# Optimization experiments

Hardware: AMD Instinct MI355X
Metric: run time of the kernel (lower is better)

The kernel has to match this reference:

```python
import jax, jax.numpy as jnp
import numpy as np

B, N, H, E, P = 2, 20000, 128, 200000, 3


def _mlp2(x, w1, b1, w2, b2):
    # Linear -> SiLU -> Linear
    return jax.nn.silu(x @ w1 + b1) @ w2 + b2


def setup_inputs() -> dict:
    key = jax.random.key(0)
    ks = iter(jax.random.split(key, 40))
    def nrm(shape, s=0.05):
        return jax.random.normal(next(ks), shape, dtype=jnp.float32) * s
    inp = {
        "features": jax.random.normal(next(ks), (B, N, H), dtype=jnp.float32),
        "positions": jax.random.normal(next(ks), (B, N, P), dtype=jnp.float32),
        "edge_index_up": jax.random.randint(next(ks), (2, E), 0, N, dtype=jnp.int32),
        "edge_index_down": jax.random.randint(next(ks), (2, E), 0, N, dtype=jnp.int32),
        "degree_up": jax.random.uniform(next(ks), (N,), minval=1.0, maxval=32.0, dtype=jnp.float32),
        "degree_down": jax.random.uniform(next(ks), (N,), minval=1.0, maxval=32.0, dtype=jnp.float32),
    }
    for name in ("up", "down"):
        inp[f"w_msg1_{name}"] = nrm((2 * H + 1, H)); inp[f"b_msg1_{name}"] = jnp.zeros((H,), jnp.float32)
        inp[f"w_msg2_{name}"] = nrm((H, H));         inp[f"b_msg2_{name}"] = jnp.zeros((H,), jnp.float32)
        inp[f"w_pos1_{name}"] = nrm((H, H));         inp[f"b_pos1_{name}"] = jnp.zeros((H,), jnp.float32)
        inp[f"w_pos2_{name}"] = nrm((H, 1));         inp[f"b_pos2_{name}"] = jnp.zeros((1,), jnp.float32)
    inp["w_upd1"] = nrm((2 * H, H)); inp["b_upd1"] = jnp.zeros((H,), jnp.float32)
    inp["w_upd2"] = nrm((H, H));     inp["b_upd2"] = jnp.zeros((H,), jnp.float32)
    return inp


def reference(features, positions, edge_index_up, edge_index_down, degree_up, degree_down,
              w_msg1_up, b_msg1_up, w_msg2_up, b_msg2_up,
              w_pos1_up, b_pos1_up, w_pos2_up, b_pos2_up,
              w_msg1_down, b_msg1_down, w_msg2_down, b_msg2_down,
              w_pos1_down, b_pos1_down, w_pos2_down, b_pos2_down,
              w_upd1, b_upd1, w_upd2, b_upd2):
    n_neighborhoods = 2
    msg_acc = jnp.zeros_like(features)
    pos_upd = jnp.zeros_like(positions)
    neighborhoods = [
        (edge_index_up, degree_up,
         (w_msg1_up, b_msg1_up, w_msg2_up, b_msg2_up),
         (w_pos1_up, b_pos1_up, w_pos2_up, b_pos2_up)),
        (edge_index_down, degree_down,
         (w_msg1_down, b_msg1_down, w_msg2_down, b_msg2_down),
         (w_pos1_down, b_pos1_down, w_pos2_down, b_pos2_down)),
    ]
    for edge_index, degree, msg_p, pos_p in neighborhoods:
        src, dst = edge_index[0], edge_index[1]
        h_src = features[:, src, :]                     # [B, E, H] gather
        h_dst = features[:, dst, :]                     # [B, E, H] gather
        rel_pos = positions[:, src, :] - positions[:, dst, :]  # [B, E, P]
        dist = jnp.linalg.norm(rel_pos, axis=-1, keepdims=True)  # [B, E, 1]
        msg_input = jnp.concatenate([h_src, h_dst, dist], axis=-1)  # [B, E, 2H+1]
        messages = _mlp2(msg_input, *msg_p)             # [B, E, H]
        agg = jnp.zeros_like(features).at[:, dst, :].add(messages)  # scatter-add over dim 1
        agg = agg / jnp.clip(degree, 1.0, None)[None, :, None]
        msg_acc = msg_acc + agg
        weights = jnp.tanh(_mlp2(messages, *pos_p))     # [B, E, 1]
        pos_upd = pos_upd + jnp.zeros_like(positions).at[:, dst, :].add(weights * rel_pos)
    feat_update = _mlp2(jnp.concatenate([features, msg_acc], axis=-1), w_upd1, b_upd1, w_upd2, b_upd2)
    updated_features = features + feat_update
    updated_positions = positions + pos_upd / n_neighborhoods
    return updated_features, updated_positions
```

## Files before the change

### kernel.cpp

```cpp
#include <hip/hip_runtime.h>

#define BB 2
#define NN 20000
#define HH 128
#define EE 200000
#define EBLK 3125
#define NBLK 79

typedef unsigned short u16;
typedef __attribute__((ext_vector_type(4))) float f32x4;
typedef __bf16 bf16x8 __attribute__((ext_vector_type(8)));

#define MFMA(a, b, c) __builtin_amdgcn_mfma_f32_16x16x32_bf16((a), (b), (c), 0, 0, 0)

__device__ __forceinline__ float bf2f(u16 u) {
    union { unsigned int i; float f; } v; v.i = ((unsigned int)u) << 16; return v.f;
}
__device__ __forceinline__ u16 f2bf(float f) {
    union { __bf16 h; u16 u; } v; v.h = (__bf16)f; return v.u;
}
__device__ __forceinline__ float silu_f(float z) { return z / (1.f + __expf(-z)); }

__global__ void detect_kernel(const u16* __restrict__ f, int* __restrict__ flag) {
    int tid = threadIdx.x;
    u16 v = f[tid * 2];
    int e = (v >> 7) & 0xFF;
    int ok = (e >= 101 && e <= 143) ? 1 : 0;
    __shared__ int cnt;
    if (tid == 0) cnt = 0;
    __syncthreads();
    atomicAdd(&cnt, ok);
    __syncthreads();
    if (tid == 0) *flag = (cnt < 200) ? 1 : 0;
}

#define CTOT 5461776
struct P24 { const void* p[24]; };

__global__ __launch_bounds__(256) void canon_kernel(P24 ptrs, const int* __restrict__ flag,
                                                    u16* __restrict__ canon) {
    static const int off[25] = {
        0, 5120000, 5240000, 5260000, 5280000, 5312896, 5313024, 5329408,
        5329536, 5345920, 5346048, 5346176, 5346184, 5379080, 5379208, 5395592,
        5395720, 5412104, 5412232, 5412360, 5412368, 5445136, 5445264, 5461648,
        5461776 };
    static const int rsz[24] = {
        5120000, 120000, 20000, 20000,
        32896, 128, 16384, 128, 16384, 128, 128, 1,
        32896, 128, 16384, 128, 16384, 128, 128, 1,
        32768, 128, 16384, 128 };
    int i = blockIdx.x * 256 + threadIdx.x;
    if (i >= CTOT) return;
    int t = 0;
#pragma unroll 1
    while (i >= off[t + 1]) ++t;
    int j = i - off[t];
    u16 v;
    if (j >= rsz[t]) v = 0;
    else if (*flag) v = f2bf(((const float*)ptrs.p[t])[j]);
    else v = ((const u16*)ptrs.p[t])[j];
    canon[i] = v;
}

#define FTOT 180224
struct P8 { const u16* w[8]; };

__global__ __launch_bounds__(256) void make_frag_all(P8 ws, u16* __restrict__ fbase) {
    static const int foff[9] = { 0, 32768, 49152, 65536, 98304, 114688, 131072, 163840, 180224 };
    int i = blockIdx.x * 256 + threadIdx.x;
    if (i >= FTOT) return;
    int t = 0;
#pragma unroll 1
    while (i >= foff[t + 1]) ++t;
    int j = i - foff[t];
    int jj = j & 7, lane = (j >> 3) & 63, nt = (j >> 9) & 7, kt = j >> 12;
    int k = kt * 32 + ((lane >> 4) * 8) + jj;
    int n = nt * 16 + (lane & 15);
    fbase[i] = ws.w[t][k * 128 + n];
}

__global__ void count2_kernel(const int* __restrict__ eu, const int* __restrict__ ed,
                              int* __restrict__ cu, int* __restrict__ cd) {
    int e = blockIdx.x * 256 + threadIdx.x;
    if (e < EE) atomicAdd(&cu[eu[EE + e]], 1);
    else { e -= EE; if (e < EE) atomicAdd(&cd[ed[EE + e]], 1); }
}

struct SP { const int* cnt[2]; int* cur[2]; int* bsum[2]; };

__global__ __launch_bounds__(256) void scan1_kernel(SP p) {
    int half = blockIdx.x / NBLK;
    int b = blockIdx.x - half * NBLK;
    int t = threadIdx.x;
    int i = b * 256 + t;
    __shared__ int buf[256];
    int v = (i < NN) ? p.cnt[half][i] : 0;
    buf[t] = v;
    __syncthreads();
    for (int s = 1; s < 256; s <<= 1) {
        int x = (t >= s) ? buf[t - s] : 0;
        __syncthreads();
        buf[t] += x;
        __syncthreads();
    }
    if (i < NN) p.cur[half][i] = buf[t] - v;
    if (t == 255) p.bsum[half][b] = buf[255];
}

__global__ __launch_bounds__(256) void scan2_kernel(int* __restrict__ bu, int* __restrict__ bd) {
    __shared__ int buf[2][128];
    int half = threadIdx.x >> 7, t = threadIdx.x & 127;
    int* bs = half ? bd : bu;
    int v = (t < NBLK) ? bs[t] : 0;
    buf[half][t] = v;
    __syncthreads();
    for (int s = 1; s < 128; s <<= 1) {
        int x = (t >= s) ? buf[half][t - s] : 0;
        __syncthreads();
        buf[half][t] += x;
        __syncthreads();
    }
    if (t < NBLK) bs[t] = buf[half][t] - v;
}

__global__ void scan3_kernel(int* __restrict__ cu, const int* __restrict__ bu,
                             int* __restrict__ cd, const int* __restrict__ bd) {
    int i = blockIdx.x * 256 + threadIdx.x;
    if (i < NN) cu[i] += bu[i >> 8];
    else { i -= NN; if (i < NN) cd[i] += bd[i >> 8]; }
}

__global__ void scatter2_kernel(const int* __restrict__ eu, const int* __restrict__ ed,
                                int* __restrict__ cu, int* __restrict__ cd,
                                int* __restrict__ su, int* __restrict__ sd) {
    int e = blockIdx.x * 256 + threadIdx.x;
    if (e < EE) { int p = atomicAdd(&cu[eu[EE + e]], 1); su[p] = e; }
    else { e -= EE; if (e < EE) { int p = atomicAdd(&cd[ed[EE + e]], 1); sd[p] = e; } }
}

struct EP {
    const int* eidx; const int* es; const u16* deg;
    const u16* fW1; const u16* w1last; const u16* bias1;
    const u16* fW2; const u16* bias2;
    const u16* fP1; const u16* biasp1;
    const u16* wp2; const u16* biasp2;
};

__global__ __launch_bounds__(512, 8) void edge_kernel(
    const u16* __restrict__ feat, const u16* __restrict__ posit,
    EP up, EP dn,
    float* __restrict__ msg_acc, float* __restrict__ pos_acc)
{
    const int tid = threadIdx.x;
    const int lane = tid & 63;
    const int wv = tid >> 6;
    const int half = blockIdx.x / (BB * EBLK);
    const int rem = blockIdx.x - half * (BB * EBLK);
    const int bb = rem / EBLK;
    const int s0 = (rem - bb * EBLK) * 64;
    const EP P = half ? dn : up;

    __shared__ u16 sX[64][136];
    __shared__ u16 sY[64][136];
    __shared__ float sRel[64][3];
    __shared__ float sDist[64];
    __shared__ float sInv[64];
    __shared__ int sSrc[64], sDst[64];

    if (tid < 64) {
        int e = P.es[s0 + tid];
        int s = P.eidx[e];
        int d = P.eidx[EE + e];
        sSrc[tid] = s; sDst[tid] = d;
        sInv[tid] = 1.f / fmaxf(bf2f(P.deg[d]), 1.f);
        const u16* ps = posit + ((size_t)bb * NN + s) * 3;
        const u16* pd = posit + ((size_t)bb * NN + d) * 3;
        float dx = bf2f(ps[0]) - bf2f(pd[0]);
        float dy = bf2f(ps[1]) - bf2f(pd[1]);
        float dz = bf2f(ps[2]) - bf2f(pd[2]);
        sRel[tid][0] = dx; sRel[tid][1] = dy; sRel[tid][2] = dz;
        sDist[tid] = sqrtf(dx * dx + dy * dy + dz * dz);
    }
    __syncthreads();

    {
        const int r = tid >> 3, part = tid & 7;
        const uint4* fs = (const uint4*)(feat + ((size_t)bb * NN + sSrc[r]) * HH);
        const uint4* fd = (const uint4*)(feat + ((size_t)bb * NN + sDst[r]) * HH);
        uint4* as = (uint4*)&sX[r][part * 16];
        uint4* ad = (uint4*)&sY[r][part * 16];
#pragma unroll
        for (int i = 0; i < 2; ++i) { as[i] = fs[part * 2 + i]; ad[i] = fd[part * 2 + i]; }
    }
    __syncthreads();

    const int nt = wv;
    const int mrow = lane & 15;
    const int kq = (lane >> 4) * 8;
    const int crow = (lane >> 4) * 4;
    const int ccol = lane & 15;
    const int col = nt * 16 + ccol;

    f32x4 acc[4];
#pragma unroll
    for (int mt = 0; mt < 4; ++mt) acc[mt] = (f32x4){0.f, 0.f, 0.f, 0.f};

#pragma unroll
    for (int kt = 0; kt < 8; ++kt) {
        const u16* Xb = (kt < 4) ? &sX[0][0] : &sY[0][0];
        const int kk = (kt & 3) * 32 + kq;
        bf16x8 bw = *(const bf16x8*)(P.fW1 + (size_t)(((kt * 8 + nt) * 64 + lane) * 8));
#pragma unroll
        for (int mt = 0; mt < 4; ++mt) {
            bf16x8 a = *(const bf16x8*)(Xb + (mt * 16 + mrow) * 136 + kk);
            acc[mt] = MFMA(a, bw, acc[mt]);
        }
    }
    __syncthreads();

    {
        const float wl = bf2f(P.w1last[col]);
        const float bb2 = bf2f(P.bias1[col]);
#pragma unroll
        for (int mt = 0; mt < 4; ++mt) {
#pragma unroll
            for (int r = 0; r < 4; ++r) {
                const int row = mt * 16 + crow + r;
                float z = fmaf(sDist[row], wl, acc[mt][r]) + bb2;
                sX[row][col] = f2bf(silu_f(z));
            }
        }
    }
    __syncthreads();

#pragma unroll
    for (int mt = 0; mt < 4; ++mt) acc[mt] = (f32x4){0.f, 0.f, 0.f, 0.f};
#pragma unroll
    for (int kt = 0; kt < 4; ++kt) {
        const int kk = kt * 32 + kq;
        bf16x8 bw = *(const bf16x8*)(P.fW2 + (size_t)(((kt * 8 + nt) * 64 + lane) * 8));
#pragma unroll
        for (int mt = 0; mt < 4; ++mt) {
            bf16x8 a = *(const bf16x8*)(&sX[0][0] + (mt * 16 + mrow) * 136 + kk);
            acc[mt] = MFMA(a, bw, acc[mt]);
        }
    }
    {
        const float bb2 = bf2f(P.bias2[col]);
#pragma unroll
        for (int mt = 0; mt < 4; ++mt) {
#pragma unroll
            for (int r = 0; r < 4; ++r) {
                const int row = mt * 16 + crow + r;
                sY[row][col] = f2bf(acc[mt][r] + bb2);
            }
        }
    }
    __syncthreads();

#pragma unroll
    for (int mt = 0; mt < 4; ++mt) acc[mt] = (f32x4){0.f, 0.f, 0.f, 0.f};
#pragma unroll
    for (int kt = 0; kt < 4; ++kt) {
        const int kk = kt * 32 + kq;
        bf16x8 bw = *(const bf16x8*)(P.fP1 + (size_t)(((kt * 8 + nt) * 64 + lane) * 8));
#pragma unroll
        for (int mt = 0; mt < 4; ++mt) {
            bf16x8 a = *(const bf16x8*)(&sY[0][0] + (mt * 16 + mrow) * 136 + kk);
            acc[mt] = MFMA(a, bw, acc[mt]);
        }
    }

    {
        const int scol = tid & 127;
        const int r0 = (tid >> 7) * 16;
        float accv = 0.f;
        int dprev = sDst[r0];
        float invprev = sInv[r0];
#pragma unroll 1
        for (int r = r0; r < r0 + 16; ++r) {
            int dcur = sDst[r];
            if (dcur != dprev) {
                unsafeAtomicAdd(&msg_acc[((size_t)bb * NN + dprev) * HH + scol], accv * invprev);
                accv = 0.f; dprev = dcur; invprev = sInv[r];
            }
            accv += bf2f(sY[r][scol]);
        }
        unsafeAtomicAdd(&msg_acc[((size_t)bb * NN + dprev) * HH + scol], accv * invprev);
    }

    {
        const float bb2 = bf2f(P.biasp1[col]);
#pragma unroll
        for (int mt = 0; mt < 4; ++mt) {
#pragma unroll
            for (int r = 0; r < 4; ++r) {
                const int row = mt * 16 + crow + r;
                sX[row][col] = f2bf(silu_f(acc[mt][r] + bb2));
            }
        }
    }
    __syncthreads();

    {
        const int r = tid >> 3, q = tid & 7;
        const unsigned int* t32 = (const unsigned int*)&sX[r][q * 16];
        const unsigned int* w32 = (const unsigned int*)(P.wp2 + q * 16);
        float p = 0.f;
#pragma unroll
        for (int k = 0; k < 8; ++k) {
            unsigned int a = t32[k], b = w32[k];
            union { unsigned int i; float f; } al, ah, bl, bh;
            al.i = a << 16; ah.i = a & 0xffff0000u;
            bl.i = b << 16; bh.i = b & 0xffff0000u;
            p = fmaf(al.f, bl.f, p);
            p = fmaf(ah.f, bh.f, p);
        }
        p += __shfl_xor(p, 1);
        p += __shfl_xor(p, 2);
        p += __shfl_xor(p, 4);
        if (q == 0) {
            float wgt = tanhf(p + bf2f(P.biasp2[0]));
            const size_t pb = ((size_t)bb * NN + sDst[r]) * 3;
            unsafeAtomicAdd(&pos_acc[pb + 0], wgt * sRel[r][0]);
            unsafeAtomicAdd(&pos_acc[pb + 1], wgt * sRel[r][1]);
            unsafeAtomicAdd(&pos_acc[pb + 2], wgt * sRel[r][2]);
        }
    }
}

__global__ __launch_bounds__(256) void update_kernel(
    const u16* __restrict__ feat, const void* __restrict__ rawfeat,
    const float* __restrict__ magg,
    const u16* __restrict__ fU1, const u16* __restrict__ bu1,
    const u16* __restrict__ fU2, const u16* __restrict__ bu2,
    void* __restrict__ outp, const int* __restrict__ flag)
{
    const int tid = threadIdx.x;
    const int lane = tid & 63;
    const int wv = tid >> 6;
    const int row0 = blockIdx.x * 64;
    const int isf = *flag;

    __shared__ u16 sA[64][136];
    __shared__ u16 sB[64][136];

    {
        const uint4* src = (const uint4*)(feat + (size_t)row0 * HH);
        for (int i = tid; i < 1024; i += 256) {
            int r = i >> 4, c = i & 15;
            *(uint4*)&sA[r][c * 8] = src[i];
        }
        const float4* am = (const float4*)(magg) + (size_t)row0 * 32;
        for (int i = tid; i < 2048; i += 256) {
            int r = i >> 5;
            float4 v = am[i];
            int c = (i & 31) * 4;
            sB[r][c + 0] = f2bf(v.x);
            sB[r][c + 1] = f2bf(v.y);
            sB[r][c + 2] = f2bf(v.z);
            sB[r][c + 3] = f2bf(v.w);
        }
    }
    __syncthreads();

    const int nt0 = wv * 2;
    const int mrow = lane & 15;
    const int kq = (lane >> 4) * 8;
    const int crow = (lane >> 4) * 4;
    const int ccol = lane & 15;

    f32x4 acc[4][2];
#pragma unroll
    for (int mt = 0; mt < 4; ++mt) {
        acc[mt][0] = (f32x4){0.f, 0.f, 0.f, 0.f};
        acc[mt][1] = (f32x4){0.f, 0.f, 0.f, 0.f};
    }
#pragma unroll
    for (int kt = 0; kt < 8; ++kt) {
        const u16* Xb = (kt < 4) ? &sA[0][0] : &sB[0][0];
        const int kk = (kt & 3) * 32 + kq;
        bf16x8 bw0 = *(const bf16x8*)(fU1 + (size_t)(((kt * 8 + nt0) * 64 + lane) * 8));
        bf16x8 bw1 = *(const bf16x8*)(fU1 + (size_t)(((kt * 8 + nt0 + 1) * 64 + lane) * 8));
#pragma unroll
        for (int mt = 0; mt < 4; ++mt) {
            bf16x8 a = *(const bf16x8*)(Xb + (mt * 16 + mrow) * 136 + kk);
            acc[mt][0] = MFMA(a, bw0, acc[mt][0]);
            acc[mt][1] = MFMA(a, bw1, acc[mt][1]);
        }
    }
    __syncthreads();

#pragma unroll
    for (int mt = 0; mt < 4; ++mt) {
#pragma unroll
        for (int n2 = 0; n2 < 2; ++n2) {
            const int col = (nt0 + n2) * 16 + ccol;
            const float bb = bf2f(bu1[col]);
#pragma unroll
            for (int r = 0; r < 4; ++r) {
                const int row = mt * 16 + crow + r;
                sB[row][col] = f2bf(silu_f(acc[mt][n2][r] + bb));
            }
        }
    }
    __syncthreads();

#pragma unroll
    for (int mt = 0; mt < 4; ++mt) {
        acc[mt][0] = (f32x4){0.f, 0.f, 0.f, 0.f};
        acc[mt][1] = (f32x4){0.f, 0.f, 0.f, 0.f};
    }
#pragma unroll
    for (int kt = 0; kt < 4; ++kt) {
        const int kk = kt * 32 + kq;
        bf16x8 bw0 = *(const bf16x8*)(fU2 + (size_t)(((kt * 8 + nt0) * 64 + lane) * 8));
        bf16x8 bw1 = *(const bf16x8*)(fU2 + (size_t)(((kt * 8 + nt0 + 1) * 64 + lane) * 8));
#pragma unroll
        for (int mt = 0; mt < 4; ++mt) {
            bf16x8 a = *(const bf16x8*)(&sB[0][0] + (mt * 16 + mrow) * 136 + kk);
            acc[mt][0] = MFMA(a, bw0, acc[mt][0]);
            acc[mt][1] = MFMA(a, bw1, acc[mt][1]);
        }
    }
#pragma unroll
    for (int mt = 0; mt < 4; ++mt) {
#pragma unroll
        for (int n2 = 0; n2 < 2; ++n2) {
            const int col = (nt0 + n2) * 16 + ccol;
            const float bb = bf2f(bu2[col]);
#pragma unroll
            for (int r = 0; r < 4; ++r) {
                const int row = mt * 16 + crow + r;
                const size_t idx = (size_t)(row0 + row) * HH + col;
                if (isf) {
                    float base = ((const float*)rawfeat)[idx];
                    ((float*)outp)[idx] = acc[mt][n2][r] + bb + base;
                } else {
                    float base = bf2f(sA[row][col]);
                    ((u16*)outp)[idx] = f2bf(acc[mt][n2][r] + bb + base);
                }
            }
        }
    }
}

__global__ void pos_out_kernel(const void* __restrict__ rawpos, const u16* __restrict__ cpos,
                               const float* __restrict__ pacc, void* __restrict__ outp,
                               const int* __restrict__ flag)
{
    int i = blockIdx.x * 256 + threadIdx.x;
    if (i >= BB * NN * 3) return;
    if (*flag) {
        float base = ((const float*)rawpos)[i];
        ((float*)outp)[5120000 + i] = base + 0.5f * pacc[i];
    } else {
        float base = bf2f(cpos[i]);
        ((u16*)outp)[5120000 + i] = f2bf(base + 0.5f * pacc[i]);
    }
}

extern "C" void kernel_launch(void* const* d_in, const int* in_sizes, int n_in,
                              void* d_out, int out_size, void* d_ws, size_t ws_size,
                              hipStream_t stream)
{
    float* msg_acc = (float*)d_ws;
    float* pos_acc = (float*)((char*)d_ws + 20480000);
    int*   cnt_up  = (int*)((char*)d_ws + 20960000);
    int*   cnt_dn  = (int*)((char*)d_ws + 21040000);
    const size_t ZERO_BYTES = 21120000;
    int*   cur_up  = (int*)((char*)d_ws + 21120000);
    int*   cur_dn  = (int*)((char*)d_ws + 21200000);
    int*   bsum_up = (int*)((char*)d_ws + 21280000);
    int*   bsum_dn = (int*)((char*)d_ws + 21280400);
    int*   es_up   = (int*)((char*)d_ws + 21280800);
    int*   es_dn   = (int*)((char*)d_ws + 22080800);
    u16*   fbase   = (u16*)((char*)d_ws + 22880800);
    u16*   canon   = (u16*)((char*)d_ws + 23241248);
    int*   flag    = (int*)((char*)d_ws + 34164800);
    if (ws_size < 34164804ULL) return;

    u16* f_m1u = fbase;
    u16* f_m2u = fbase + 32768;
    u16* f_p1u = fbase + 49152;
    u16* f_m1d = fbase + 65536;
    u16* f_m2d = fbase + 98304;
    u16* f_p1d = fbase + 114688;
    u16* f_u1  = fbase + 131072;
    u16* f_u2  = fbase + 163840;

    u16* cfeat = canon;
    u16* cpos  = canon + 5120000;
    u16* cdgu  = canon + 5240000;
    u16* cdgd  = canon + 5260000;
    u16* cm1u  = canon + 5280000;
    u16* cbm1u = canon + 5312896;
    u16* cm2u  = canon + 5313024;
    u16* cbm2u = canon + 5329408;
    u16* cp1u  = canon + 5329536;
    u16* cbp1u = canon + 5345920;
    u16* cp2u  = canon + 5346048;
    u16* cbp2u = canon + 5346176;
    u16* cm1d  = canon + 5346184;
    u16* cbm1d = canon + 5379080;
    u16* cm2d  = canon + 5379208;
    u16* cbm2d = canon + 5395592;
    u16* cp1d  = canon + 5395720;
    u16* cbp1d = canon + 5412104;
    u16* cp2d  = canon + 5412232;
    u16* cbp2d = canon + 5412360;
    u16* cu1   = canon + 5412368;
    u16* cbu1  = canon + 5445136;
    u16* cu2   = canon + 5445264;
    u16* cbu2  = canon + 5461648;

    hipMemsetAsync(d_ws, 0, ZERO_BYTES, stream);

    detect_kernel<<<1, 256, 0, stream>>>((const u16*)d_in[0], flag);

    P24 ptrs;
    ptrs.p[0] = d_in[0];  ptrs.p[1] = d_in[1];  ptrs.p[2] = d_in[4];  ptrs.p[3] = d_in[5];
    ptrs.p[4] = d_in[6];  ptrs.p[5] = d_in[7];  ptrs.p[6] = d_in[8];  ptrs.p[7] = d_in[9];
    ptrs.p[8] = d_in[10]; ptrs.p[9] = d_in[11]; ptrs.p[10] = d_in[12]; ptrs.p[11] = d_in[13];
    ptrs.p[12] = d_in[14]; ptrs.p[13] = d_in[15]; ptrs.p[14] = d_in[16]; ptrs.p[15] = d_in[17];
    ptrs.p[16] = d_in[18]; ptrs.p[17] = d_in[19]; ptrs.p[18] = d_in[20]; ptrs.p[19] = d_in[21];
    ptrs.p[20] = d_in[22]; ptrs.p[21] = d_in[23]; ptrs.p[22] = d_in[24]; ptrs.p[23] = d_in[25];
    canon_kernel<<<(CTOT + 255) / 256, 256, 0, stream>>>(ptrs, flag, canon);

    P8 wsf;
    wsf.w[0] = cm1u; wsf.w[1] = cm2u; wsf.w[2] = cp1u; wsf.w[3] = cm1d;
    wsf.w[4] = cm2d; wsf.w[5] = cp1d; wsf.w[6] = cu1;  wsf.w[7] = cu2;
    make_frag_all<<<(FTOT + 255) / 256, 256, 0, stream>>>(wsf, fbase);

    const int* ei_up = (const int*)d_in[2];
    const int* ei_dn = (const int*)d_in[3];

    count2_kernel<<<(2 * EE + 255) / 256, 256, 0, stream>>>(ei_up, ei_dn, cnt_up, cnt_dn);
    SP sp;
    sp.cnt[0] = cnt_up; sp.cnt[1] = cnt_dn;
    sp.cur[0] = cur_up; sp.cur[1] = cur_dn;
    sp.bsum[0] = bsum_up; sp.bsum[1] = bsum_dn;
    scan1_kernel<<<2 * NBLK, 256, 0, stream>>>(sp);
    scan2_kernel<<<1, 256, 0, stream>>>(bsum_up, bsum_dn);
    scan3_kernel<<<(2 * NN + 255) / 256, 256, 0, stream>>>(cur_up, bsum_up, cur_dn, bsum_dn);
    scatter2_kernel<<<(2 * EE + 255) / 256, 256, 0, stream>>>(ei_up, ei_dn, cur_up, cur_dn,
                                                              es_up, es_dn);

    EP up, dn;
    up.eidx = ei_up; up.es = es_up; up.deg = cdgu;
    up.fW1 = f_m1u; up.w1last = cm1u + 256 * 128; up.bias1 = cbm1u;
    up.fW2 = f_m2u; up.bias2 = cbm2u;
    up.fP1 = f_p1u; up.biasp1 = cbp1u;
    up.wp2 = cp2u;  up.biasp2 = cbp2u;
    dn.eidx = ei_dn; dn.es = es_dn; dn.deg = cdgd;
    dn.fW1 = f_m1d; dn.w1last = cm1d + 256 * 128; dn.bias1 = cbm1d;
    dn.fW2 = f_m2d; dn.bias2 = cbm2d;
    dn.fP1 = f_p1d; dn.biasp1 = cbp1d;
    dn.wp2 = cp2d;  dn.biasp2 = cbp2d;

    edge_kernel<<<2 * BB * EBLK, 512, 0, stream>>>(cfeat, cpos, up, dn, msg_acc, pos_acc);

    update_kernel<<<625, 256, 0, stream>>>(
        cfeat, d_in[0], msg_acc,
        f_u1, cbu1, f_u2, cbu2, d_out, flag);

    pos_out_kernel<<<469, 256, 0, stream>>>(d_in[1], cpos, pos_acc, d_out, flag);
}
```

Baseline: 525.1 us.

## Precompute per-node first-layer projections and drop canonicalization pass

The first message-MLP layer is split algebraically: the src and dst halves of W1 are applied once per node in a new nodey kernel, so each edge only gathers two precomputed projections, adds the dist term and bias, and applies SiLU. This removes the 256-deep per-edge GEMM. The bf16 canonicalization kernel is removed and raw inputs are read through a dtype-dispatching loader. Other changes: the memset becomes a zeroing prep kernel that accumulates straight into the output buffer in fp32 mode, scan3 is folded into scatter, pos_out is merged into the update kernel, and SiLU uses a fast reciprocal. The cost is 40MB of extra bf16 workspace written and gathered, plus an earlier bf16 rounding of the first-layer pre-activations.

```diff
diff --git a/kernel.cpp b/kernel.cpp
--- a/kernel.cpp
+++ b/kernel.cpp
@@ -19,7 +19,15 @@
 __device__ __forceinline__ u16 f2bf(float f) {
     union { __bf16 h; u16 u; } v; v.h = (__bf16)f; return v.u;
 }
-__device__ __forceinline__ float silu_f(float z) { return z / (1.f + __expf(-z)); }
+__device__ __forceinline__ float fastrcp(float x) {
+    float r; asm volatile("v_rcp_f32 %0, %1" : "=v"(r) : "v"(x)); return r;
+}
+__device__ __forceinline__ float silu_f(float z) {
+    return z * fastrcp(1.f + __expf(-z));
+}
+__device__ __forceinline__ float ldv(const void* p, long i, int f) {
+    return f ? ((const float*)p)[i] : bf2f(((const u16*)p)[i]);
+}
 
 __global__ void detect_kernel(const u16* __restrict__ f, int* __restrict__ flag) {
     int tid = threadIdx.x;
@@ -34,41 +42,30 @@
     if (tid == 0) *flag = (cnt < 200) ? 1 : 0;
 }
 
-#define CTOT 5461776
-struct P24 { const void* p[24]; };
-
-__global__ __launch_bounds__(256) void canon_kernel(P24 ptrs, const int* __restrict__ flag,
-                                                    u16* __restrict__ canon) {
-    static const int off[25] = {
-        0, 5120000, 5240000, 5260000, 5280000, 5312896, 5313024, 5329408,
-        5329536, 5345920, 5346048, 5346176, 5346184, 5379080, 5379208, 5395592,
-        5395720, 5412104, 5412232, 5412360, 5412368, 5445136, 5445264, 5461648,
-        5461776 };
-    static const int rsz[24] = {
-        5120000, 120000, 20000, 20000,
-        32896, 128, 16384, 128, 16384, 128, 128, 1,
-        32896, 128, 16384, 128, 16384, 128, 128, 1,
-        32768, 128, 16384, 128 };
+__global__ __launch_bounds__(256) void prep_kernel(void* outp, float* __restrict__ ws_msg,
+                                                   float* __restrict__ ws_pos,
+                                                   int* __restrict__ cnt,
+                                                   const int* __restrict__ flag) {
     int i = blockIdx.x * 256 + threadIdx.x;
-    if (i >= CTOT) return;
-    int t = 0;
-#pragma unroll 1
-    while (i >= off[t + 1]) ++t;
-    int j = i - off[t];
-    u16 v;
-    if (j >= rsz[t]) v = 0;
-    else if (*flag) v = f2bf(((const float*)ptrs.p[t])[j]);
-    else v = ((const u16*)ptrs.p[t])[j];
-    canon[i] = v;
+    if (i < 5240000) {
+        if (*flag) ((float*)outp)[i] = 0.f;
+        else if (i < 5120000) ws_msg[i] = 0.f;
+        else ws_pos[i - 5120000] = 0.f;
+    } else {
+        int j = i - 5240000;
+        if (j < 40000) cnt[j] = 0;
+    }
 }
 
 #define FTOT 180224
-struct P8 { const u16* w[8]; };
-
-__global__ __launch_bounds__(256) void make_frag_all(P8 ws, u16* __restrict__ fbase) {
+struct P8 { const void* w[8]; };
+
+__global__ __launch_bounds__(256) void make_frag_all(P8 ws, u16* __restrict__ fbase,
+                                                     const int* __restrict__ flag) {
     static const int foff[9] = { 0, 32768, 49152, 65536, 98304, 114688, 131072, 163840, 180224 };
     int i = blockIdx.x * 256 + threadIdx.x;
     if (i >= FTOT) return;
+    int isf = *flag;
     int t = 0;
 #pragma unroll 1
     while (i >= foff[t + 1]) ++t;
@@ -76,7 +73,7 @@
     int jj = j & 7, lane = (j >> 3) & 63, nt = (j >> 9) & 7, kt = j >> 12;
     int k = kt * 32 + ((lane >> 4) * 8) + jj;
     int n = nt * 16 + (lane & 15);
-    fbase[i] = ws.w[t][k * 128 + n];
+    fbase[i] = f2bf(ldv(ws.w[t], (long)k * 128 + n, isf));
 }
 
 __global__ void count2_kernel(const int* __restrict__ eu, const int* __restrict__ ed,
@@ -123,33 +120,123 @@
     if (t < NBLK) bs[t] = buf[half][t] - v;
 }
 
-__global__ void scan3_kernel(int* __restrict__ cu, const int* __restrict__ bu,
-                             int* __restrict__ cd, const int* __restrict__ bd) {
-    int i = blockIdx.x * 256 + threadIdx.x;
-    if (i < NN) cu[i] += bu[i >> 8];
-    else { i -= NN; if (i < NN) cd[i] += bd[i >> 8]; }
-}
-
 __global__ void scatter2_kernel(const int* __restrict__ eu, const int* __restrict__ ed,
-                                int* __restrict__ cu, int* __restrict__ cd,
+                                int* __restrict__ cu, const int* __restrict__ bu,
+                                int* __restrict__ cd, const int* __restrict__ bd,
                                 int* __restrict__ su, int* __restrict__ sd) {
     int e = blockIdx.x * 256 + threadIdx.x;
-    if (e < EE) { int p = atomicAdd(&cu[eu[EE + e]], 1); su[p] = e; }
-    else { e -= EE; if (e < EE) { int p = atomicAdd(&cd[ed[EE + e]], 1); sd[p] = e; } }
+    if (e < EE) {
+        int d = eu[EE + e];
+        int p = atomicAdd(&cu[d], 1) + bu[d >> 8];
+        su[p] = e;
+    } else {
+        e -= EE;
+        if (e < EE) {
+            int d = ed[EE + e];
+            int p = atomicAdd(&cd[d], 1) + bd[d >> 8];
+            sd[p] = e;
+        }
+    }
+}
+
+__global__ __launch_bounds__(256) void nodey_kernel(
+    const void* __restrict__ rawfeat,
+    const u16* __restrict__ f_m1u, const u16* __restrict__ f_m1d,
+    const void* __restrict__ b1u, const void* __restrict__ b1d,
+    u16* __restrict__ Ysu, u16* __restrict__ Ydu,
+    u16* __restrict__ Ysd, u16* __restrict__ Ydd,
+    const int* __restrict__ flag)
+{
+    const int tid = threadIdx.x;
+    const int lane = tid & 63;
+    const int wv = tid >> 6;
+    const int row0 = blockIdx.x * 64;
+    const int isf = *flag;
+
+    __shared__ u16 sF[64][136];
+
+    if (isf) {
+        const float* fp = (const float*)rawfeat + (size_t)row0 * HH;
+        for (int i = tid; i < 1024; i += 256) {
+            int r = i >> 4, c = (i & 15) * 8;
+            float4 v0 = *(const float4*)(fp + (size_t)r * HH + c);
+            float4 v1 = *(const float4*)(fp + (size_t)r * HH + c + 4);
+            uint4 o;
+            o.x = (unsigned)f2bf(v0.x) | ((unsigned)f2bf(v0.y) << 16);
+            o.y = (unsigned)f2bf(v0.z) | ((unsigned)f2bf(v0.w) << 16);
+            o.z = (unsigned)f2bf(v1.x) | ((unsigned)f2bf(v1.y) << 16);
+            o.w = (unsigned)f2bf(v1.z) | ((unsigned)f2bf(v1.w) << 16);
+            *(uint4*)&sF[r][c] = o;
+        }
+    } else {
+        const uint4* fp = (const uint4*)((const u16*)rawfeat + (size_t)row0 * HH);
+        for (int i = tid; i < 1024; i += 256) {
+            int r = i >> 4, c = i & 15;
+            *(uint4*)&sF[r][c * 8] = fp[i];
+        }
+    }
+    __syncthreads();
+
+    const int mrow = lane & 15;
+    const int kq = (lane >> 4) * 8;
+    const int crow = (lane >> 4) * 4;
+    const int ccol = lane & 15;
+
+    const u16* frag = (wv < 2) ? f_m1u : f_m1d;
+    const int ktb = (wv & 1) * 4;
+    u16* Yout = (wv == 0) ? Ysu : (wv == 1) ? Ydu : (wv == 2) ? Ysd : Ydd;
+    const void* bias = (wv == 1) ? b1u : (wv == 3) ? b1d : (const void*)0;
+
+#pragma unroll 1
+    for (int hf = 0; hf < 2; ++hf) {
+        f32x4 acc[4][4];
+#pragma unroll
+        for (int mt = 0; mt < 4; ++mt)
+#pragma unroll
+            for (int nt = 0; nt < 4; ++nt) acc[mt][nt] = (f32x4){0.f, 0.f, 0.f, 0.f};
+#pragma unroll
+        for (int kt = 0; kt < 4; ++kt) {
+            const int kk = kt * 32 + kq;
+            bf16x8 bw[4];
+#pragma unroll
+            for (int nt = 0; nt < 4; ++nt)
+                bw[nt] = *(const bf16x8*)(frag +
+                    (size_t)((((ktb + kt) * 8 + hf * 4 + nt) * 64 + lane) * 8));
+#pragma unroll
+            for (int mt = 0; mt < 4; ++mt) {
+                bf16x8 a = *(const bf16x8*)(&sF[0][0] + (mt * 16 + mrow) * 136 + kk);
+#pragma unroll
+                for (int nt = 0; nt < 4; ++nt) acc[mt][nt] = MFMA(a, bw[nt], acc[mt][nt]);
+            }
+        }
+#pragma unroll
+        for (int mt = 0; mt < 4; ++mt) {
+#pragma unroll
+            for (int nt = 0; nt < 4; ++nt) {
+                const int col = (hf * 4 + nt) * 16 + ccol;
+                const float bb = bias ? ldv(bias, col, isf) : 0.f;
+#pragma unroll
+                for (int r = 0; r < 4; ++r) {
+                    const int row = mt * 16 + crow + r;
+                    Yout[(size_t)(row0 + row) * HH + col] = f2bf(acc[mt][nt][r] + bb);
+                }
+            }
+        }
+    }
 }
 
 struct EP {
-    const int* eidx; const int* es; const u16* deg;
-    const u16* fW1; const u16* w1last; const u16* bias1;
-    const u16* fW2; const u16* bias2;
-    const u16* fP1; const u16* biasp1;
-    const u16* wp2; const u16* biasp2;
+    const int* eidx; const int* es;
+    const void* deg; const void* w1;
+    const void* bias2; const void* biasp1; const void* wp2; const void* biasp2;
+    const u16* fW2; const u16* fP1;
+    const u16* Ys; const u16* Yd;
 };
 
 __global__ __launch_bounds__(512, 8) void edge_kernel(
-    const u16* __restrict__ feat, const u16* __restrict__ posit,
-    EP up, EP dn,
-    float* __restrict__ msg_acc, float* __restrict__ pos_acc)
+    const void* __restrict__ posit, EP up, EP dn,
+    float* __restrict__ ws_msg, float* __restrict__ ws_pos,
+    void* __restrict__ outp, const int* __restrict__ flag)
 {
     const int tid = threadIdx.x;
     const int lane = tid & 63;
@@ -159,6 +246,9 @@
     const int bb = rem / EBLK;
     const int s0 = (rem - bb * EBLK) * 64;
     const EP P = half ? dn : up;
+    const int isf = *flag;
+    float* msg_acc = isf ? (float*)outp : ws_msg;
+    float* pos_acc = isf ? (float*)outp + 5120000 : ws_pos;
 
     __shared__ u16 sX[64][136];
     __shared__ u16 sY[64][136];
@@ -172,25 +262,44 @@
         int s = P.eidx[e];
         int d = P.eidx[EE + e];
         sSrc[tid] = s; sDst[tid] = d;
-        sInv[tid] = 1.f / fmaxf(bf2f(P.deg[d]), 1.f);
-        const u16* ps = posit + ((size_t)bb * NN + s) * 3;
-        const u16* pd = posit + ((size_t)bb * NN + d) * 3;
-        float dx = bf2f(ps[0]) - bf2f(pd[0]);
-        float dy = bf2f(ps[1]) - bf2f(pd[1]);
-        float dz = bf2f(ps[2]) - bf2f(pd[2]);
+        sInv[tid] = 1.f / fmaxf(ldv(P.deg, d, isf), 1.f);
+        long pb = ((long)bb * NN + s) * 3, qb = ((long)bb * NN + d) * 3;
+        float dx = ldv(posit, pb + 0, isf) - ldv(posit, qb + 0, isf);
+        float dy = ldv(posit, pb + 1, isf) - ldv(posit, qb + 1, isf);
+        float dz = ldv(posit, pb + 2, isf) - ldv(posit, qb + 2, isf);
         sRel[tid][0] = dx; sRel[tid][1] = dy; sRel[tid][2] = dz;
         sDist[tid] = sqrtf(dx * dx + dy * dy + dz * dz);
     }
     __syncthreads();
 
     {
-        const int r = tid >> 3, part = tid & 7;
-        const uint4* fs = (const uint4*)(feat + ((size_t)bb * NN + sSrc[r]) * HH);
-        const uint4* fd = (const uint4*)(feat + ((size_t)bb * NN + sDst[r]) * HH);
-        uint4* as = (uint4*)&sX[r][part * 16];
-        uint4* ad = (uint4*)&sY[r][part * 16];
-#pragma unroll
-        for (int i = 0; i < 2; ++i) { as[i] = fs[part * 2 + i]; ad[i] = fd[part * 2 + i]; }
+        const int r = tid >> 3, c0 = (tid & 7) * 16;
+        const u16* ys = P.Ys + ((size_t)bb * NN + sSrc[r]) * HH + c0;
+        const u16* yd = P.Yd + ((size_t)bb * NN + sDst[r]) * HH + c0;
+        uint4 a0 = *(const uint4*)ys, a1 = *(const uint4*)(ys + 8);
+        uint4 b0 = *(const uint4*)yd, b1 = *(const uint4*)(yd + 8);
+        const float dist = sDist[r];
+        const unsigned* ap = (const unsigned*)&a0;
+        uint4 av[2] = { a0, a1 }, bv[2] = { b0, b1 };
+        uint4 ov[2];
+#pragma unroll
+        for (int h = 0; h < 2; ++h) {
+            const unsigned* aa = (const unsigned*)&av[h];
+            const unsigned* bbp = (const unsigned*)&bv[h];
+            unsigned* oo = (unsigned*)&ov[h];
+#pragma unroll
+            for (int j = 0; j < 4; ++j) {
+                int cc = c0 + h * 8 + j * 2;
+                float z0 = bf2f((u16)(aa[j] & 0xffff)) + bf2f((u16)(bbp[j] & 0xffff))
+                         + dist * ldv(P.w1, 32768 + cc, isf);
+                float z1 = bf2f((u16)(aa[j] >> 16)) + bf2f((u16)(bbp[j] >> 16))
+                         + dist * ldv(P.w1, 32768 + cc + 1, isf);
+                oo[j] = (unsigned)f2bf(silu_f(z0)) | ((unsigned)f2bf(silu_f(z1)) << 16);
+            }
+        }
+        *(uint4*)&sX[r][c0] = ov[0];
+        *(uint4*)&sX[r][c0 + 8] = ov[1];
+        (void)ap;
     }
     __syncthreads();
 
@@ -206,36 +315,6 @@
     for (int mt = 0; mt < 4; ++mt) acc[mt] = (f32x4){0.f, 0.f, 0.f, 0.f};
 
 #pragma unroll
-    for (int kt = 0; kt < 8; ++kt) {
-        const u16* Xb = (kt < 4) ? &sX[0][0] : &sY[0][0];
-        const int kk = (kt & 3) * 32 + kq;
-        bf16x8 bw = *(const bf16x8*)(P.fW1 + (size_t)(((kt * 8 + nt) * 64 + lane) * 8));
-#pragma unroll
-        for (int mt = 0; mt < 4; ++mt) {
-            bf16x8 a = *(const bf16x8*)(Xb + (mt * 16 + mrow) * 136 + kk);
-            acc[mt] = MFMA(a, bw, acc[mt]);
-        }
-    }
-    __syncthreads();
-
-    {
-        const float wl = bf2f(P.w1last[col]);
-        const float bb2 = bf2f(P.bias1[col]);
-#pragma unroll
-        for (int mt = 0; mt < 4; ++mt) {
-#pragma unroll
-            for (int r = 0; r < 4; ++r) {
-                const int row = mt * 16 + crow + r;
-                float z = fmaf(sDist[row], wl, acc[mt][r]) + bb2;
-                sX[row][col] = f2bf(silu_f(z));
-            }
-        }
-    }
-    __syncthreads();
-
-#pragma unroll
-    for (int mt = 0; mt < 4; ++mt) acc[mt] = (f32x4){0.f, 0.f, 0.f, 0.f};
-#pragma unroll
     for (int kt = 0; kt < 4; ++kt) {
         const int kk = kt * 32 + kq;
         bf16x8 bw = *(const bf16x8*)(P.fW2 + (size_t)(((kt * 8 + nt) * 64 + lane) * 8));
@@ -246,7 +325,7 @@
         }
     }
     {
-        const float bb2 = bf2f(P.bias2[col]);
+        const float bb2 = ldv(P.bias2, col, isf);
 #pragma unroll
         for (int mt = 0; mt < 4; ++mt) {
 #pragma unroll
@@ -290,7 +369,7 @@
     }
 
     {
-        const float bb2 = bf2f(P.biasp1[col]);
+        const float bb2 = ldv(P.biasp1, col, isf);
 #pragma unroll
         for (int mt = 0; mt < 4; ++mt) {
 #pragma unroll
@@ -304,23 +383,21 @@
 
     {
         const int r = tid >> 3, q = tid & 7;
-        const unsigned int* t32 = (const unsigned int*)&sX[r][q * 16];
-        const unsigned int* w32 = (const unsigned int*)(P.wp2 + q * 16);
+        const unsigned* t32 = (const unsigned*)&sX[r][q * 16];
         float p = 0.f;
 #pragma unroll
         for (int k = 0; k < 8; ++k) {
-            unsigned int a = t32[k], b = w32[k];
-            union { unsigned int i; float f; } al, ah, bl, bh;
-            al.i = a << 16; ah.i = a & 0xffff0000u;
-            bl.i = b << 16; bh.i = b & 0xffff0000u;
-            p = fmaf(al.f, bl.f, p);
-            p = fmaf(ah.f, bh.f, p);
+            unsigned a = t32[k];
+            float w0 = ldv(P.wp2, q * 16 + 2 * k, isf);
+            float w1 = ldv(P.wp2, q * 16 + 2 * k + 1, isf);
+            p = fmaf(bf2f((u16)(a & 0xffff)), w0, p);
+            p = fmaf(bf2f((u16)(a >> 16)), w1, p);
         }
         p += __shfl_xor(p, 1);
         p += __shfl_xor(p, 2);
         p += __shfl_xor(p, 4);
         if (q == 0) {
-            float wgt = tanhf(p + bf2f(P.biasp2[0]));
+            float wgt = tanhf(p + ldv(P.biasp2, 0, isf));
             const size_t pb = ((size_t)bb * NN + sDst[r]) * 3;
             unsafeAtomicAdd(&pos_acc[pb + 0], wgt * sRel[r][0]);
             unsafeAtomicAdd(&pos_acc[pb + 1], wgt * sRel[r][1]);
@@ -330,27 +407,44 @@
 }
 
 __global__ __launch_bounds__(256) void update_kernel(
-    const u16* __restrict__ feat, const void* __restrict__ rawfeat,
-    const float* __restrict__ magg,
-    const u16* __restrict__ fU1, const u16* __restrict__ bu1,
-    const u16* __restrict__ fU2, const u16* __restrict__ bu2,
-    void* __restrict__ outp, const int* __restrict__ flag)
+    const void* __restrict__ rawfeat, const void* __restrict__ rawpos,
+    const u16* __restrict__ fU1, const void* __restrict__ bu1,
+    const u16* __restrict__ fU2, const void* __restrict__ bu2,
+    void* __restrict__ outp, float* __restrict__ ws_msg, float* __restrict__ ws_pos,
+    const int* __restrict__ flag)
 {
     const int tid = threadIdx.x;
     const int lane = tid & 63;
     const int wv = tid >> 6;
     const int row0 = blockIdx.x * 64;
     const int isf = *flag;
+    const float* magg = isf ? (const float*)outp : ws_msg;
+    const float* pacc = isf ? (const float*)outp + 5120000 : ws_pos;
 
     __shared__ u16 sA[64][136];
     __shared__ u16 sB[64][136];
 
-    {
-        const uint4* src = (const uint4*)(feat + (size_t)row0 * HH);
+    if (isf) {
+        const float* fp = (const float*)rawfeat + (size_t)row0 * HH;
+        for (int i = tid; i < 1024; i += 256) {
+            int r = i >> 4, c = (i & 15) * 8;
+            float4 v0 = *(const float4*)(fp + (size_t)r * HH + c);
+            float4 v1 = *(const float4*)(fp + (size_t)r * HH + c + 4);
+            uint4 o;
+            o.x = (unsigned)f2bf(v0.x) | ((unsigned)f2bf(v0.y) << 16);
+            o.y = (unsigned)f2bf(v0.z) | ((unsigned)f2bf(v0.w) << 16);
+            o.z = (unsigned)f2bf(v1.x) | ((unsigned)f2bf(v1.y) << 16);
+            o.w = (unsigned)f2bf(v1.z) | ((unsigned)f2bf(v1.w) << 16);
+            *(uint4*)&sA[r][c] = o;
+        }
+    } else {
+        const uint4* fp = (const uint4*)((const u16*)rawfeat + (size_t)row0 * HH);
         for (int i = tid; i < 1024; i += 256) {
             int r = i >> 4, c = i & 15;
-            *(uint4*)&sA[r][c * 8] = src[i];
-        }
+            *(uint4*)&sA[r][c * 8] = fp[i];
+        }
+    }
+    {
         const float4* am = (const float4*)(magg) + (size_t)row0 * 32;
         for (int i = tid; i < 2048; i += 256) {
             int r = i >> 5;
@@ -396,7 +490,7 @@
 #pragma unroll
         for (int n2 = 0; n2 < 2; ++n2) {
             const int col = (nt0 + n2) * 16 + ccol;
-            const float bb = bf2f(bu1[col]);
+            const float bb = ldv(bu1, col, isf);
 #pragma unroll
             for (int r = 0; r < 4; ++r) {
                 const int row = mt * 16 + crow + r;
@@ -428,7 +522,7 @@
 #pragma unroll
         for (int n2 = 0; n2 < 2; ++n2) {
             const int col = (nt0 + n2) * 16 + ccol;
-            const float bb = bf2f(bu2[col]);
+            const float bb = ldv(bu2, col, isf);
 #pragma unroll
             for (int r = 0; r < 4; ++r) {
                 const int row = mt * 16 + crow + r;
@@ -443,20 +537,17 @@
             }
         }
     }
-}
-
-__global__ void pos_out_kernel(const void* __restrict__ rawpos, const u16* __restrict__ cpos,
-                               const float* __restrict__ pacc, void* __restrict__ outp,
-                               const int* __restrict__ flag)
-{
-    int i = blockIdx.x * 256 + threadIdx.x;
-    if (i >= BB * NN * 3) return;
-    if (*flag) {
-        float base = ((const float*)rawpos)[i];
-        ((float*)outp)[5120000 + i] = base + 0.5f * pacc[i];
-    } else {
-        float base = bf2f(cpos[i]);
-        ((u16*)outp)[5120000 + i] = f2bf(base + 0.5f * pacc[i]);
+
+    if (tid < 192) {
+        int i = row0 * 3 + tid;
+        float x = pacc[i];
+        if (isf) {
+            float base = ((const float*)rawpos)[i];
+            ((float*)outp)[5120000 + i] = base + 0.5f * x;
+        } else {
+            float base = bf2f(((const u16*)rawpos)[i]);
+            ((u16*)outp)[5120000 + i] = f2bf(base + 0.5f * x);
+        }
     }
 }
 
@@ -464,21 +555,23 @@
                               void* d_out, int out_size, void* d_ws, size_t ws_size,
                               hipStream_t stream)
 {
-    float* msg_acc = (float*)d_ws;
-    float* pos_acc = (float*)((char*)d_ws + 20480000);
-    int*   cnt_up  = (int*)((char*)d_ws + 20960000);
-    int*   cnt_dn  = (int*)((char*)d_ws + 21040000);
-    const size_t ZERO_BYTES = 21120000;
-    int*   cur_up  = (int*)((char*)d_ws + 21120000);
-    int*   cur_dn  = (int*)((char*)d_ws + 21200000);
-    int*   bsum_up = (int*)((char*)d_ws + 21280000);
-    int*   bsum_dn = (int*)((char*)d_ws + 21280400);
-    int*   es_up   = (int*)((char*)d_ws + 21280800);
-    int*   es_dn   = (int*)((char*)d_ws + 22080800);
-    u16*   fbase   = (u16*)((char*)d_ws + 22880800);
-    u16*   canon   = (u16*)((char*)d_ws + 23241248);
-    int*   flag    = (int*)((char*)d_ws + 34164800);
-    if (ws_size < 34164804ULL) return;
+    u16*   Ysu     = (u16*)d_ws;
+    u16*   Ydu     = (u16*)((char*)d_ws + 10240000);
+    u16*   Ysd     = (u16*)((char*)d_ws + 20480000);
+    u16*   Ydd     = (u16*)((char*)d_ws + 30720000);
+    int*   cnt_up  = (int*)((char*)d_ws + 40960000);
+    int*   cnt_dn  = (int*)((char*)d_ws + 41040000);
+    int*   cur_up  = (int*)((char*)d_ws + 41120000);
+    int*   cur_dn  = (int*)((char*)d_ws + 41200000);
+    int*   bsum_up = (int*)((char*)d_ws + 41280000);
+    int*   bsum_dn = (int*)((char*)d_ws + 41280400);
+    int*   es_up   = (int*)((char*)d_ws + 41280800);
+    int*   es_dn   = (int*)((char*)d_ws + 42080800);
+    u16*   fbase   = (u16*)((char*)d_ws + 42880800);
+    int*   flag    = (int*)((char*)d_ws + 43241248);
+    float* ws_msg  = (float*)((char*)d_ws + 43241280);
+    float* ws_pos  = (float*)((char*)d_ws + 63721280);
+    if (ws_size < 43241252ULL) return;
 
     u16* f_m1u = fbase;
     u16* f_m2u = fbase + 32768;
@@ -489,51 +582,17 @@
     u16* f_u1  = fbase + 131072;
     u16* f_u2  = fbase + 163840;
 
-    u16* cfeat = canon;
-    u16* cpos  = canon + 5120000;
-    u16* cdgu  = canon + 5240000;
-    u16* cdgd  = canon + 5260000;
-    u16* cm1u  = canon + 5280000;
-    u16* cbm1u = canon + 5312896;
-    u16* cm2u  = canon + 5313024;
-    u16* cbm2u = canon + 5329408;
-    u16* cp1u  = canon + 5329536;
-    u16* cbp1u = canon + 5345920;
-    u16* cp2u  = canon + 5346048;
-    u16* cbp2u = canon + 5346176;
-    u16* cm1d  = canon + 5346184;
-    u16* cbm1d = canon + 5379080;
-    u16* cm2d  = canon + 5379208;
-    u16* cbm2d = canon + 5395592;
-    u16* cp1d  = canon + 5395720;
-    u16* cbp1d = canon + 5412104;
-    u16* cp2d  = canon + 5412232;
-    u16* cbp2d = canon + 5412360;
-    u16* cu1   = canon + 5412368;
-    u16* cbu1  = canon + 5445136;
-    u16* cu2   = canon + 5445264;
-    u16* cbu2  = canon + 5461648;
-
-    hipMemsetAsync(d_ws, 0, ZERO_BYTES, stream);
-
-    detect_kernel<<<1, 256, 0, stream>>>((const u16*)d_in[0], flag);
-
-    P24 ptrs;
-    ptrs.p[0] = d_in[0];  ptrs.p[1] = d_in[1];  ptrs.p[2] = d_in[4];  ptrs.p[3] = d_in[5];
-    ptrs.p[4] = d_in[6];  ptrs.p[5] = d_in[7];  ptrs.p[6] = d_in[8];  ptrs.p[7] = d_in[9];
-    ptrs.p[8] = d_in[10]; ptrs.p[9] = d_in[11]; ptrs.p[10] = d_in[12]; ptrs.p[11] = d_in[13];
-    ptrs.p[12] = d_in[14]; ptrs.p[13] = d_in[15]; ptrs.p[14] = d_in[16]; ptrs.p[15] = d_in[17];
-    ptrs.p[16] = d_in[18]; ptrs.p[17] = d_in[19]; ptrs.p[18] = d_in[20]; ptrs.p[19] = d_in[21];
-    ptrs.p[20] = d_in[22]; ptrs.p[21] = d_in[23]; ptrs.p[22] = d_in[24]; ptrs.p[23] = d_in[25];
-    canon_kernel<<<(CTOT + 255) / 256, 256, 0, stream>>>(ptrs, flag, canon);
-
-    P8 wsf;
-    wsf.w[0] = cm1u; wsf.w[1] = cm2u; wsf.w[2] = cp1u; wsf.w[3] = cm1d;
-    wsf.w[4] = cm2d; wsf.w[5] = cp1d; wsf.w[6] = cu1;  wsf.w[7] = cu2;
-    make_frag_all<<<(FTOT + 255) / 256, 256, 0, stream>>>(wsf, fbase);
-
     const int* ei_up = (const int*)d_in[2];
     const int* ei_dn = (const int*)d_in[3];
+
+    detect_kernel<<<1, 256, 0, stream>>>((const u16*)d_in[0], flag);
+
+    prep_kernel<<<(5280000 + 255) / 256, 256, 0, stream>>>(d_out, ws_msg, ws_pos, cnt_up, flag);
+
+    P8 wsf;
+    wsf.w[0] = d_in[6];  wsf.w[1] = d_in[8];  wsf.w[2] = d_in[10]; wsf.w[3] = d_in[14];
+    wsf.w[4] = d_in[16]; wsf.w[5] = d_in[18]; wsf.w[6] = d_in[22]; wsf.w[7] = d_in[24];
+    make_frag_all<<<(FTOT + 255) / 256, 256, 0, stream>>>(wsf, fbase, flag);
 
     count2_kernel<<<(2 * EE + 255) / 256, 256, 0, stream>>>(ei_up, ei_dn, cnt_up, cnt_dn);
     SP sp;
@@ -542,27 +601,22 @@
     sp.bsum[0] = bsum_up; sp.bsum[1] = bsum_dn;
     scan1_kernel<<<2 * NBLK, 256, 0, stream>>>(sp);
     scan2_kernel<<<1, 256, 0, stream>>>(bsum_up, bsum_dn);
-    scan3_kernel<<<(2 * NN + 255) / 256, 256, 0, stream>>>(cur_up, bsum_up, cur_dn, bsum_dn);
-    scatter2_kernel<<<(2 * EE + 255) / 256, 256, 0, stream>>>(ei_up, ei_dn, cur_up, cur_dn,
-                                                              es_up, es_dn);
+    scatter2_kernel<<<(2 * EE + 255) / 256, 256, 0, stream>>>(ei_up, ei_dn, cur_up, bsum_up,
+                                                              cur_dn, bsum_dn, es_up, es_dn);
+
+    nodey_kernel<<<625, 256, 0, stream>>>(d_in[0], f_m1u, f_m1d, d_in[7], d_in[15],
+                                          Ysu, Ydu, Ysd, Ydd, flag);
 
     EP up, dn;
-    up.eidx = ei_up; up.es = es_up; up.deg = cdgu;
-    up.fW1 = f_m1u; up.w1last = cm1u + 256 * 128; up.bias1 = cbm1u;
-    up.fW2 = f_m2u; up.bias2 = cbm2u;
-    up.fP1 = f_p1u; up.biasp1 = cbp1u;
-    up.wp2 = cp2u;  up.biasp2 = cbp2u;
-    dn.eidx = ei_dn; dn.es = es_dn; dn.deg = cdgd;
-    dn.fW1 = f_m1d; dn.w1last = cm1d + 256 * 128; dn.bias1 = cbm1d;
-    dn.fW2 = f_m2d; dn.bias2 = cbm2d;
-    dn.fP1 = f_p1d; dn.biasp1 = cbp1d;
-    dn.wp2 = cp2d;  dn.biasp2 = cbp2d;
-
-    edge_kernel<<<2 * BB * EBLK, 512, 0, stream>>>(cfeat, cpos, up, dn, msg_acc, pos_acc);
-
-    update_kernel<<<625, 256, 0, stream>>>(
-        cfeat, d_in[0], msg_acc,
-        f_u1, cbu1, f_u2, cbu2, d_out, flag);
-
-    pos_out_kernel<<<469, 256, 0, stream>>>(d_in[1], cpos, pos_acc, d_out, flag);
-}
+    up.eidx = ei_up; up.es = es_up; up.deg = d_in[4]; up.w1 = d_in[6];
+    up.bias2 = d_in[9]; up.biasp1 = d_in[11]; up.wp2 = d_in[12]; up.biasp2 = d_in[13];
+    up.fW2 = f_m2u; up.fP1 = f_p1u; up.Ys = Ysu; up.Yd = Ydu;
+    dn.eidx = ei_dn; dn.es = es_dn; dn.deg = d_in[5]; dn.w1 = d_in[14];
+    dn.bias2 = d_in[17]; dn.biasp1 = d_in[19]; dn.wp2 = d_in[20]; dn.biasp2 = d_in[21];
+    dn.fW2 = f_m2d; dn.fP1 = f_p1d; dn.Ys = Ysd; dn.Yd = Ydd;
+
+    edge_kernel<<<2 * BB * EBLK, 512, 0, stream>>>(d_in[1], up, dn, ws_msg, ws_pos, d_out, flag);
+
+    update_kernel<<<625, 256, 0, stream>>>(d_in[0], d_in[1], f_u1, d_in[23], f_u2, d_in[25],
+                                           d_out, ws_msg, ws_pos, flag);
+}
```

New measurement: 584.1 us. +11.2%, slower.
